# Kernel tuning notes

Measured on AMD Instinct MI355X. Metric: run time of the kernel, lower is better.

The kernel has to match this reference:

```python
import jax, jax.numpy as jnp
import numpy as np

MUL = 32            # multiplicity of 0e and 1o irreps
IN_DIM = MUL * 4    # 32 scalars + 32 vectors = 128
SH_DIM = 4          # 1x0e + 1x1o
N_EDGE_FEAT = 128
HIDDEN = 128
W_NUMEL = 4 * MUL * MUL  # 4 CG paths, uvw weights 32x1x32 each
EPS = 1e-5
INV_SQRT3 = 1.0 / np.sqrt(3.0)
PATH_NORM = 1.0 / np.sqrt(2.0 * MUL)  # 2 paths per output irrep, fan-in MUL


def _fc(edge_attr, W1, b1, W2, b2):
    h = jax.nn.relu(edge_attr @ W1 + b1)
    return h @ W2 + b2  # [E, W_NUMEL]


def _tensor_product(x, sh, w):
    # FullyConnectedTensorProduct for (32x0e+32x1o) x (1x0e+1x1o) -> (32x0e+32x1o)
    # CG (real w3j): 0x0->0: 1 ; 0x1->1, 1x0->1, 1x1->0: delta/sqrt(3)
    E = x.shape[0]
    x0 = x[:, :MUL]                      # [E,32]   scalars
    x1 = x[:, MUL:].reshape(E, MUL, 3)   # [E,32,3] vectors
    sh0 = sh[:, 0]                       # [E]
    sh1 = sh[:, 1:4]                     # [E,3]
    wA = w[:, 0 * MUL * MUL:1 * MUL * MUL].reshape(E, MUL, MUL)  # 0e x 0e -> 0e
    wB = w[:, 1 * MUL * MUL:2 * MUL * MUL].reshape(E, MUL, MUL)  # 0e x 1o -> 1o
    wC = w[:, 2 * MUL * MUL:3 * MUL * MUL].reshape(E, MUL, MUL)  # 1o x 0e -> 1o
    wD = w[:, 3 * MUL * MUL:4 * MUL * MUL].reshape(E, MUL, MUL)  # 1o x 1o -> 0e
    out0 = PATH_NORM * (
        jnp.einsum('eu,euw->ew', x0 * sh0[:, None], wA)
        + INV_SQRT3 * jnp.einsum('eui,ei,euw->ew', x1, sh1, wD))
    out1 = PATH_NORM * INV_SQRT3 * (
        jnp.einsum('eu,ei,euw->ewi', x0, sh1, wB)
        + jnp.einsum('eui,euw->ewi', x1 * sh0[:, None, None], wC))
    return jnp.concatenate([out0, out1.reshape(E, MUL * 3)], axis=-1)  # [E,128]


def _batch_norm(x, bn_weight, bn_bias):
    # e3nn-style equivariant BatchNorm (training stats): scalars get mean/var
    # normalization + affine; vectors get norm normalization + scale.
    N = x.shape[0]
    s = x[:, :MUL]                       # [N,32]
    v = x[:, MUL:].reshape(N, MUL, 3)    # [N,32,3]
    s = s - s.mean(axis=0)
    s = s * (jax.lax.rsqrt((s ** 2).mean(axis=0) + EPS) * bn_weight[:MUL]) + bn_bias
    v_norm = jax.lax.rsqrt((v ** 2).mean(axis=-1).mean(axis=0) + EPS)  # [32]
    v = v * (v_norm * bn_weight[MUL:])[None, :, None]
    return jnp.concatenate([s, v.reshape(N, MUL * 3)], axis=-1)


def _forward(node_attr, edge_index, edge_attr, edge_sh,
             W1, b1, W2, b2, bn_weight, bn_bias):
    edge_src, edge_dst = edge_index[0], edge_index[1]
    N = node_attr.shape[0]
    w = _fc(edge_attr, W1, b1, W2, b2)                     # [E, 4096]
    tp = _tensor_product(node_attr[edge_dst], edge_sh, w)  # [E, 128]
    # scatter mean over edge_src
    summed = jax.ops.segment_sum(tp, edge_src, num_segments=N)
    counts = jax.ops.segment_sum(jnp.ones((tp.shape[0],), tp.dtype), edge_src,
                                 num_segments=N)
    out = summed / jnp.maximum(counts, 1.0)[:, None]
    out = out + node_attr                                  # residual (same dim, pad=0)
    return _batch_norm(out, bn_weight, bn_bias)


def setup_inputs() -> dict:
    key = jax.random.key(0)
    ks = jax.random.split(key, 10)
    N, E = 10000, 60000
    node_attr = jax.random.normal(ks[0], (N, IN_DIM), jnp.float32)
    edge_index = jax.random.randint(ks[1], (2, E), 0, N)
    edge_attr = jax.random.normal(ks[2], (E, N_EDGE_FEAT), jnp.float32)
    edge_sh = jax.random.normal(ks[3], (E, SH_DIM), jnp.float32)
    W1 = jax.random.normal(ks[4], (N_EDGE_FEAT, HIDDEN), jnp.float32) / np.sqrt(N_EDGE_FEAT)
    b1 = jnp.zeros((HIDDEN,), jnp.float32)
    W2 = jax.random.normal(ks[5], (HIDDEN, W_NUMEL), jnp.float32) / np.sqrt(HIDDEN)
    b2 = jnp.zeros((W_NUMEL,), jnp.float32)
    bn_weight = jnp.ones((2 * MUL,), jnp.float32)
    bn_bias = jnp.zeros((MUL,), jnp.float32)
    return {"node_attr": node_attr, "edge_index": edge_index,
            "edge_attr": edge_attr, "edge_sh": edge_sh,
            "W1": W1, "b1": b1, "W2": W2, "b2": b2,
            "bn_weight": bn_weight, "bn_bias": bn_bias}


def reference(node_attr, edge_index, edge_attr, edge_sh,
              W1, b1, W2, b2, bn_weight, bn_bias):
    return _forward(node_attr, edge_index, edge_attr, edge_sh,
                    W1, b1, W2, b2, bn_weight, bn_bias)
```

## Files before the change

### kernel.cpp

```cpp
#include <hip/hip_runtime.h>
#include <math.h>

#define EPSV 1e-5f
#define IS3  0.57735026918962576f
#define PNRM 0.125f

typedef __attribute__((ext_vector_type(8)))  short  short8;
typedef __attribute__((ext_vector_type(16))) float  floatx16;

static __device__ inline unsigned short f2bf(float f) {
    unsigned int u = __float_as_uint(f);
    return (unsigned short)((u + 0x7fff + ((u >> 16) & 1)) >> 16);
}
static __device__ inline float bflo(unsigned int u) { return __uint_as_float(u << 16); }
static __device__ inline float bfhi(unsigned int u) { return __uint_as_float(u & 0xffff0000u); }

#define GLD16(gp, lp) __builtin_amdgcn_global_load_lds( \
    (const __attribute__((address_space(1))) unsigned int*)(gp), \
    (__attribute__((address_space(3))) unsigned int*)(lp), 16, 0, 0)

__global__ __launch_bounds__(256) void k0_tile(const float* __restrict__ W2,
                                               const float* __restrict__ W1,
                                               unsigned short* __restrict__ W2T,
                                               unsigned short* __restrict__ W1T,
                                               const int* __restrict__ ei,
                                               int* __restrict__ deg, int E) {
    const int bx = blockIdx.x, tid = threadIdx.x;
    if (bx >= 132) {
        int e = (bx - 132) * 256 + tid;
        if (e < E) atomicAdd(&deg[ei[e]], 1);
        return;
    }
    __shared__ float tile[128 * 33];
    const float* src;
    unsigned short* dst;
    int nc, tb;
    if (bx < 128) { src = W2; dst = W2T; nc = 4096; tb = bx; }
    else          { src = W1; dst = W1T; nc = 128;  tb = bx - 128; }
    const int c0 = tb * 32;
#pragma unroll
    for (int r = 0; r < 16; ++r) {
        int lin = r * 256 + tid;
        int k = lin >> 5, c = lin & 31;
        tile[k * 33 + c] = src[(size_t)k * nc + c0 + c];
    }
    __syncthreads();
#pragma unroll
    for (int r = 0; r < 2; ++r) {
        int g = r * 256 + tid;
        int kc = g >> 5, c = g & 31;
        short8 v;
#pragma unroll
        for (int j = 0; j < 8; ++j)
            v[j] = (short)f2bf(tile[(kc * 8 + j) * 33 + c]);
        *(short8*)(dst + (size_t)tb * 4096 + kc * 256 + c * 8) = v;
    }
}

__global__ __launch_bounds__(256) void k1_fc(const float* __restrict__ ea,
                                             const unsigned short* __restrict__ W1T,
                                             const float* __restrict__ b1,
                                             unsigned short* __restrict__ hsw,
                                             const int* __restrict__ deg,
                                             int* __restrict__ rowptr,
                                             int N, int E) {
    __shared__ __align__(16) unsigned short W1s[16384];
    __shared__ __align__(16) unsigned short bounce[4 * 1056];
    const int tid = threadIdx.x, lane = tid & 63, wv = tid >> 6;
    const int half = lane >> 5, col = lane & 31;
    const int nfc = (E + 127) / 128;

    if (blockIdx.x >= nfc) {
        int* part = (int*)W1s;
        const int chunk = (N + 255) / 256;
        const int base = tid * chunk;
        int s = 0;
        for (int i = 0; i < chunk; ++i) {
            int n = base + i;
            if (n < N) s += deg[n];
        }
        part[tid] = s;
        __syncthreads();
        for (int off = 1; off < 256; off <<= 1) {
            int t = 0;
            if (tid >= off) t = part[tid - off];
            __syncthreads();
            if (tid >= off) part[tid] += t;
            __syncthreads();
        }
        int prefix = (tid == 0) ? 0 : part[tid - 1];
        for (int i = 0; i < chunk; ++i) {
            int n = base + i;
            if (n < N) { rowptr[n] = prefix; prefix += deg[n]; }
        }
        if (tid == 0) rowptr[N] = part[255];
        return;
    }

    const int e0 = blockIdx.x * 128;

#pragma unroll
    for (int q = 0; q < 8; ++q) {
        int chunk = wv * 8 + q;
        GLD16((const char*)W1T + chunk * 1024 + lane * 16, (char*)W1s + chunk * 1024);
    }

    int e = e0 + wv * 32 + col; if (e >= E) e = E - 1;
    short8 afr[8];
#pragma unroll
    for (int c = 0; c < 8; ++c) {
        const float4* p = (const float4*)(ea + (size_t)e * 128 + c * 16 + half * 8);
        float4 f0 = p[0], f1 = p[1];
        short8 v;
        v[0] = (short)f2bf(f0.x); v[1] = (short)f2bf(f0.y);
        v[2] = (short)f2bf(f0.z); v[3] = (short)f2bf(f0.w);
        v[4] = (short)f2bf(f1.x); v[5] = (short)f2bf(f1.y);
        v[6] = (short)f2bf(f1.z); v[7] = (short)f2bf(f1.w);
        afr[c] = v;
    }
    __syncthreads();

    unsigned short* myb = bounce + wv * 1056;
    const int gg = blockIdx.x * 4 + wv;
#pragma unroll
    for (int jt = 0; jt < 4; ++jt) {
        floatx16 d = {0,0,0,0,0,0,0,0,0,0,0,0,0,0,0,0};
#pragma unroll
        for (int c = 0; c < 8; ++c) {
            short8 bf = *(const short8*)((const char*)W1s + jt * 8192 + (2 * c + half) * 512 + col * 16);
            d = __builtin_amdgcn_mfma_f32_32x32x16_bf16(afr[c], bf, d, 0, 0, 0);
        }
        float b1v = b1[jt * 32 + col];
#pragma unroll
        for (int reg = 0; reg < 16; ++reg) {
            int r = (reg & 3) + 8 * (reg >> 2) + 4 * half;
            float v = d[reg] + b1v;
            v = v > 0.f ? v : 0.f;
            myb[(col >> 3) * 264 + r * 8 + (col & 7)] = f2bf(v);
        }
#pragma unroll
        for (int s = 0; s < 2; ++s) {
            short8 v = *(const short8*)&myb[(s * 2 + (lane >> 5)) * 264 + (lane & 31) * 8];
            *(short8*)(hsw + (size_t)gg * 4096 + jt * 1024 + s * 512 + lane * 8) = v;
        }
    }
}

__global__ __launch_bounds__(256, 2) void k2_mfma(const unsigned short* __restrict__ hsw,
                                                  const unsigned short* __restrict__ W2T,
                                                  const float* __restrict__ b2,
                                                  const float* __restrict__ na,
                                                  const int* __restrict__ ei,
                                                  const float* __restrict__ sh,
                                                  const int* __restrict__ rowptr,
                                                  int* __restrict__ cursor,
                                                  float* __restrict__ tp, int E) {
    __shared__ __align__(16) char smem[32768];
    __shared__ int posbuf[64];
    unsigned short* Ctb = (unsigned short*)smem;
    float* red = (float*)smem;

    const int tid = threadIdx.x, lane = tid & 63, wv = tid >> 6;
    const int half = lane >> 5, col = lane & 31;
    const int ust = wv >> 1, esub = wv & 1;
    const int e0 = blockIdx.x * 64;

    if (tid < 64) {
        int e = e0 + tid;
        if (e < E) {
            int s = ei[e];
            posbuf[tid] = rowptr[s] + atomicAdd(&cursor[s], 1);
        }
    }

    for (int idx = tid; idx < 2048; idx += 256) {
        int el = idx & 63, u = idx >> 6;
        int e = e0 + el; int ec = e < E ? e : E - 1;
        int dn = ei[E + ec];
        const float* nar = na + (size_t)dn * 128;
        float x0  = nar[u];
        float x10 = nar[32 + u * 3], x11 = nar[33 + u * 3], x12 = nar[34 + u * 3];
        const float* shr = sh + (size_t)ec * 4;
        float s0 = shr[0], s1 = shr[1], s2 = shr[2], s3 = shr[3];
        int o = u * 64 + el;
        Ctb[0 * 2048 + o] = f2bf(PNRM * x0 * s0);
        Ctb[1 * 2048 + o] = f2bf(PNRM * IS3 * x0);
        Ctb[2 * 2048 + o] = f2bf(PNRM * IS3 * s0 * x10);
        Ctb[3 * 2048 + o] = f2bf(PNRM * IS3 * s0 * x11);
        Ctb[4 * 2048 + o] = f2bf(PNRM * IS3 * s0 * x12);
        Ctb[5 * 2048 + o] = f2bf(PNRM * IS3 * (x10 * s1 + x11 * s2 + x12 * s3));
    }

    const int gg = blockIdx.x * 2 + esub;
    short8 afr[8];
#pragma unroll
    for (int c = 0; c < 8; ++c)
        afr[c] = *(const short8*)(hsw + (size_t)gg * 4096 + (2 * c + half) * 256 + col * 8);

    __syncthreads();

    float acc0[16] = {}, accB[16] = {}, accC0[16] = {}, accC1[16] = {}, accC2[16] = {};
    const int elb0 = esub * 32 + half * 4;
    const unsigned short* bbase = W2T + half * 256 + col * 8;

#define LOADB(p, br, b2r) do {                                         \
        int _ct = 2 * (p) + ust;                                       \
        const unsigned short* _bp = bbase + (size_t)_ct * 4096;        \
        _Pragma("unroll")                                              \
        for (int _c = 0; _c < 8; ++_c)                                 \
            (br)[_c] = *(const short8*)(_bp + _c * 512);               \
        (b2r) = b2[_ct * 32 + col];                                    \
    } while (0)

#define COMPUTE(p, br, b2v) do {                                                              \
        const int _ct = 2 * (p) + ust;                                                        \
        const int _b = _ct >> 5, _u = _ct & 31;                                               \
        floatx16 d = {0,0,0,0,0,0,0,0,0,0,0,0,0,0,0,0};                                       \
        _Pragma("unroll")                                                                     \
        for (int _c = 0; _c < 8; ++_c)                                                        \
            d = __builtin_amdgcn_mfma_f32_32x32x16_bf16(afr[_c], (br)[_c], d, 0, 0, 0);       \
        if (_b == 0 || _b == 3) {                                                             \
            const unsigned short* tb = Ctb + (_b == 0 ? 0 : 5) * 2048;                        \
            _Pragma("unroll")                                                                 \
            for (int q = 0; q < 4; ++q) {                                                     \
                uint2 cv = *(const uint2*)&tb[_u * 64 + elb0 + q * 8];                        \
                acc0[q * 4 + 0] += bflo(cv.x) * (d[q * 4 + 0] + (b2v));                       \
                acc0[q * 4 + 1] += bfhi(cv.x) * (d[q * 4 + 1] + (b2v));                       \
                acc0[q * 4 + 2] += bflo(cv.y) * (d[q * 4 + 2] + (b2v));                       \
                acc0[q * 4 + 3] += bfhi(cv.y) * (d[q * 4 + 3] + (b2v));                       \
            }                                                                                 \
        } else if (_b == 1) {                                                                 \
            _Pragma("unroll")                                                                 \
            for (int q = 0; q < 4; ++q) {                                                     \
                uint2 cv = *(const uint2*)&Ctb[1 * 2048 + _u * 64 + elb0 + q * 8];            \
                accB[q * 4 + 0] += bflo(cv.x) * (d[q * 4 + 0] + (b2v));                       \
                accB[q * 4 + 1] += bfhi(cv.x) * (d[q * 4 + 1] + (b2v));                       \
                accB[q * 4 + 2] += bflo(cv.y) * (d[q * 4 + 2] + (b2v));                       \
                accB[q * 4 + 3] += bfhi(cv.y) * (d[q * 4 + 3] + (b2v));                       \
            }                                                                                 \
        } else {                                                                              \
            _Pragma("unroll")                                                                 \
            for (int q = 0; q < 4; ++q) {                                                     \
                uint2 cu0 = *(const uint2*)&Ctb[2 * 2048 + _u * 64 + elb0 + q * 8];           \
                uint2 cu1 = *(const uint2*)&Ctb[3 * 2048 + _u * 64 + elb0 + q * 8];           \
                uint2 cu2 = *(const uint2*)&Ctb[4 * 2048 + _u * 64 + elb0 + q * 8];           \
                float f0[4] = {bflo(cu0.x), bfhi(cu0.x), bflo(cu0.y), bfhi(cu0.y)};           \
                float f1[4] = {bflo(cu1.x), bfhi(cu1.x), bflo(cu1.y), bfhi(cu1.y)};           \
                float f2[4] = {bflo(cu2.x), bfhi(cu2.x), bflo(cu2.y), bfhi(cu2.y)};           \
                _Pragma("unroll")                                                             \
                for (int rr = 0; rr < 4; ++rr) {                                              \
                    float v = d[q * 4 + rr] + (b2v);                                          \
                    accC0[q * 4 + rr] += f0[rr] * v;                                          \
                    accC1[q * 4 + rr] += f1[rr] * v;                                          \
                    accC2[q * 4 + rr] += f2[rr] * v;                                          \
                }                                                                             \
            }                                                                                 \
        }                                                                                     \
    } while (0)

    short8 bA[8], bB[8], bC[8];
    float b2A, b2B, b2C;
    LOADB(0, bA, b2A); LOADB(1, bB, b2B); LOADB(2, bC, b2C);
    for (int p = 0; p < 60; p += 3) {
        COMPUTE(p,     bA, b2A); LOADB(p + 3, bA, b2A);
        COMPUTE(p + 1, bB, b2B); LOADB(p + 4, bB, b2B);
        COMPUTE(p + 2, bC, b2C); LOADB(p + 5, bC, b2C);
    }
    COMPUTE(60, bA, b2A); LOADB(63, bA, b2A);
    COMPUTE(61, bB, b2B);
    COMPUTE(62, bC, b2C);
    COMPUTE(63, bA, b2A);
#undef LOADB
#undef COMPUTE

    __syncthreads();
    if (ust == 1) {
#pragma unroll
        for (int q = 0; q < 4; ++q) {
#pragma unroll
            for (int rr = 0; rr < 4; ++rr) {
                int reg = q * 4 + rr;
                int el = esub * 32 + q * 8 + half * 4 + rr;
                int e = e0 + el; int ec = e < E ? e : E - 1;
                float4 sv = *(const float4*)(sh + (size_t)ec * 4);
                red[(((esub * 4 + 0) * 16 + reg) << 6) + lane] = acc0[reg];
                red[(((esub * 4 + 1) * 16 + reg) << 6) + lane] = sv.y * accB[reg] + accC0[reg];
                red[(((esub * 4 + 2) * 16 + reg) << 6) + lane] = sv.z * accB[reg] + accC1[reg];
                red[(((esub * 4 + 3) * 16 + reg) << 6) + lane] = sv.w * accB[reg] + accC2[reg];
            }
        }
    }
    __syncthreads();
    if (ust == 0) {
#pragma unroll
        for (int q = 0; q < 4; ++q) {
#pragma unroll
            for (int rr = 0; rr < 4; ++rr) {
                int reg = q * 4 + rr;
                int el = esub * 32 + q * 8 + half * 4 + rr;
                int e = e0 + el;
                if (e >= E) continue;
                float4 sv = *(const float4*)(sh + (size_t)e * 4);
                float a0 = acc0[reg] + red[(((esub * 4 + 0) * 16 + reg) << 6) + lane];
                float o0 = sv.y * accB[reg] + accC0[reg] + red[(((esub * 4 + 1) * 16 + reg) << 6) + lane];
                float o1 = sv.z * accB[reg] + accC1[reg] + red[(((esub * 4 + 2) * 16 + reg) << 6) + lane];
                float o2 = sv.w * accB[reg] + accC2[reg] + red[(((esub * 4 + 3) * 16 + reg) << 6) + lane];
                float* tpe = tp + (size_t)posbuf[el] * 128;
                tpe[col] = a0;
                tpe[32 + col * 3 + 0] = o0;
                tpe[32 + col * 3 + 1] = o1;
                tpe[32 + col * 3 + 2] = o2;
            }
        }
    }
}

__global__ __launch_bounds__(256) void k4_gather(const float* __restrict__ tp,
                                                 const int* __restrict__ rowptr,
                                                 const float* __restrict__ na,
                                                 float* __restrict__ pre,
                                                 float* __restrict__ stats, int N) {
    __shared__ float bns[96];
    const int tid = threadIdx.x;
    if (tid < 96) bns[tid] = 0.f;
    __syncthreads();
    const int o = tid & 127, hf = tid >> 7;
    for (int n = blockIdx.x * 2 + hf; n < N; n += gridDim.x * 2) {
        int r0 = rowptr[n], r1 = rowptr[n + 1];
        float s = 0.f;
        int j = r0;
        for (; j + 4 <= r1; j += 4) {
            float t0 = tp[(size_t)(j + 0) * 128 + o];
            float t1 = tp[(size_t)(j + 1) * 128 + o];
            float t2 = tp[(size_t)(j + 2) * 128 + o];
            float t3 = tp[(size_t)(j + 3) * 128 + o];
            s += (t0 + t1) + (t2 + t3);
        }
        for (; j < r1; ++j)
            s += tp[(size_t)j * 128 + o];
        int dg = r1 - r0;
        float cf = (float)(dg > 0 ? dg : 1);
        float v = s / cf + na[(size_t)n * 128 + o];
        pre[(size_t)n * 128 + o] = v;
        if (o < 32) {
            atomicAdd(&bns[o], v);
            atomicAdd(&bns[32 + o], v * v);
        } else {
            atomicAdd(&bns[64 + (o - 32) / 3], v * v);
        }
    }
    __syncthreads();
    if (tid < 96) atomicAdd(&stats[tid], bns[tid]);
}

__global__ __launch_bounds__(256) void k5_bn(const float* __restrict__ pre,
                                             const float* __restrict__ stats,
                                             const float* __restrict__ bnw,
                                             const float* __restrict__ bnb,
                                             float* __restrict__ out, int N) {
    size_t idx = (size_t)blockIdx.x * 256 + threadIdx.x;
    if (idx >= (size_t)N * 128) return;
    int o = (int)(idx & 127);
    float v = pre[idx];
    float invN = 1.f / (float)N;
    if (o < 32) {
        float m   = stats[o] * invN;
        float var = stats[32 + o] * invN - m * m;
        out[idx] = (v - m) * rsqrtf(var + EPSV) * bnw[o] + bnb[o];
    } else {
        int j = (o - 32) / 3;
        float vn = rsqrtf(stats[64 + j] * invN * (1.f / 3.f) + EPSV);
        out[idx] = v * vn * bnw[32 + j];
    }
}

extern "C" void kernel_launch(void* const* d_in, const int* in_sizes, int n_in,
                              void* d_out, int out_size, void* d_ws, size_t ws_size,
                              hipStream_t stream) {
    const float* node_attr  = (const float*)d_in[0];
    const int*   edge_index = (const int*)d_in[1];
    const float* edge_attr  = (const float*)d_in[2];
    const float* edge_sh    = (const float*)d_in[3];
    const float* W1  = (const float*)d_in[4];
    const float* b1  = (const float*)d_in[5];
    const float* W2  = (const float*)d_in[6];
    const float* b2  = (const float*)d_in[7];
    const float* bnw = (const float*)d_in[8];
    const float* bnb = (const float*)d_in[9];

    const int N = in_sizes[0] / 128;
    const int E = in_sizes[1] / 2;
    const int ngroups = ((E + 127) / 128) * 4;

    float* tp     = (float*)d_ws;
    float* pre    = tp + (size_t)E * 128;
    float* stats  = pre + (size_t)N * 128;
    int*   deg    = (int*)(stats + 96);
    int*   cursor = deg + N;
    int*   rowptr = cursor + N;
    char* pbase = (char*)(rowptr + N + 1);
    pbase += (16 - ((size_t)pbase & 15)) & 15;
    unsigned short* hsw = (unsigned short*)pbase;
    unsigned short* W2T = hsw + (size_t)ngroups * 4096;
    unsigned short* W1T = W2T + (size_t)524288;

    hipMemsetAsync(stats, 0, (96 + 2 * (size_t)N) * sizeof(int), stream);

    k0_tile<<<132 + (E + 255) / 256, 256, 0, stream>>>(W2, W1, W2T, W1T,
                                                       edge_index, deg, E);
    k1_fc<<<(E + 127) / 128 + 1, 256, 0, stream>>>(edge_attr, W1T, b1, hsw,
                                                   deg, rowptr, N, E);
    k2_mfma<<<(E + 63) / 64, 256, 0, stream>>>(hsw, W2T, b2, node_attr, edge_index,
                                               edge_sh, rowptr, cursor, tp, E);
    k4_gather<<<1024, 256, 0, stream>>>(tp, rowptr, node_attr, pre, stats, N);
    size_t ntot = (size_t)N * 128;
    k5_bn<<<(int)((ntot + 255) / 256), 256, 0, stream>>>(pre, stats, bnw, bnb,
                                                         (float*)d_out, N);
}
```

Before: 255.7 us.

## Fuse gather and batch-norm into one cooperative kernel with grid sync

Merges the per-node gather/mean kernel and the batch-norm apply kernel into one cooperative kernel. Each thread keeps its 16 node values in registers, the block statistics are reduced, a grid-wide barrier follows, and then the normalization is applied directly from registers. This drops the intermediate pre buffer write and reread plus one launch. In exchange it depends on a 512-block cooperative launch, a grid sync, and coverage capped at 16 iterations, so correctness needs N ≤ 16384.

```diff
diff --git a/kernel.cpp b/kernel.cpp
--- a/kernel.cpp
+++ b/kernel.cpp
@@ -1,5 +1,8 @@
 #include <hip/hip_runtime.h>
+#include <hip/hip_cooperative_groups.h>
 #include <math.h>
+
+namespace cg = cooperative_groups;
 
 #define EPSV 1e-5f
 #define IS3  0.57735026918962576f
@@ -315,62 +318,70 @@
     }
 }
 
-__global__ __launch_bounds__(256) void k4_gather(const float* __restrict__ tp,
-                                                 const int* __restrict__ rowptr,
-                                                 const float* __restrict__ na,
-                                                 float* __restrict__ pre,
-                                                 float* __restrict__ stats, int N) {
+__global__ __launch_bounds__(256) void k4c_bn(const float* __restrict__ tp,
+                                              const int* __restrict__ rowptr,
+                                              const float* __restrict__ na,
+                                              float* __restrict__ stats,
+                                              const float* __restrict__ bnw,
+                                              const float* __restrict__ bnb,
+                                              float* __restrict__ out, int N) {
     __shared__ float bns[96];
     const int tid = threadIdx.x;
     if (tid < 96) bns[tid] = 0.f;
     __syncthreads();
     const int o = tid & 127, hf = tid >> 7;
-    for (int n = blockIdx.x * 2 + hf; n < N; n += gridDim.x * 2) {
-        int r0 = rowptr[n], r1 = rowptr[n + 1];
-        float s = 0.f;
-        int j = r0;
-        for (; j + 4 <= r1; j += 4) {
-            float t0 = tp[(size_t)(j + 0) * 128 + o];
-            float t1 = tp[(size_t)(j + 1) * 128 + o];
-            float t2 = tp[(size_t)(j + 2) * 128 + o];
-            float t3 = tp[(size_t)(j + 3) * 128 + o];
-            s += (t0 + t1) + (t2 + t3);
-        }
-        for (; j < r1; ++j)
-            s += tp[(size_t)j * 128 + o];
-        int dg = r1 - r0;
-        float cf = (float)(dg > 0 ? dg : 1);
-        float v = s / cf + na[(size_t)n * 128 + o];
-        pre[(size_t)n * 128 + o] = v;
-        if (o < 32) {
-            atomicAdd(&bns[o], v);
-            atomicAdd(&bns[32 + o], v * v);
-        } else {
-            atomicAdd(&bns[64 + (o - 32) / 3], v * v);
+    const int nbase = blockIdx.x * 2 + hf;
+    const int stride = gridDim.x * 2;
+    float vreg[16];
+#pragma unroll
+    for (int it = 0; it < 16; ++it) {
+        int n = nbase + it * stride;
+        if (n < N) {
+            int r0 = rowptr[n], r1 = rowptr[n + 1];
+            float s = 0.f;
+            int j = r0;
+            for (; j + 4 <= r1; j += 4) {
+                float t0 = tp[(size_t)(j + 0) * 128 + o];
+                float t1 = tp[(size_t)(j + 1) * 128 + o];
+                float t2 = tp[(size_t)(j + 2) * 128 + o];
+                float t3 = tp[(size_t)(j + 3) * 128 + o];
+                s += (t0 + t1) + (t2 + t3);
+            }
+            for (; j < r1; ++j)
+                s += tp[(size_t)j * 128 + o];
+            int dg = r1 - r0;
+            float cf = (float)(dg > 0 ? dg : 1);
+            float v = s / cf + na[(size_t)n * 128 + o];
+            vreg[it] = v;
+            if (o < 32) {
+                atomicAdd(&bns[o], v);
+                atomicAdd(&bns[32 + o], v * v);
+            } else {
+                atomicAdd(&bns[64 + (o - 32) / 3], v * v);
+            }
         }
     }
     __syncthreads();
     if (tid < 96) atomicAdd(&stats[tid], bns[tid]);
-}
-
-__global__ __launch_bounds__(256) void k5_bn(const float* __restrict__ pre,
-                                             const float* __restrict__ stats,
-                                             const float* __restrict__ bnw,
-                                             const float* __restrict__ bnb,
-                                             float* __restrict__ out, int N) {
-    size_t idx = (size_t)blockIdx.x * 256 + threadIdx.x;
-    if (idx >= (size_t)N * 128) return;
-    int o = (int)(idx & 127);
-    float v = pre[idx];
+
+    cg::this_grid().sync();
+
     float invN = 1.f / (float)N;
+    float scale, bias;
     if (o < 32) {
         float m   = stats[o] * invN;
         float var = stats[32 + o] * invN - m * m;
-        out[idx] = (v - m) * rsqrtf(var + EPSV) * bnw[o] + bnb[o];
+        float is  = rsqrtf(var + EPSV) * bnw[o];
+        scale = is; bias = bnb[o] - m * is;
     } else {
-        int j = (o - 32) / 3;
-        float vn = rsqrtf(stats[64 + j] * invN * (1.f / 3.f) + EPSV);
-        out[idx] = v * vn * bnw[32 + j];
+        int jj = (o - 32) / 3;
+        scale = rsqrtf(stats[64 + jj] * invN * (1.f / 3.f) + EPSV) * bnw[32 + jj];
+        bias = 0.f;
+    }
+#pragma unroll
+    for (int it = 0; it < 16; ++it) {
+        int n = nbase + it * stride;
+        if (n < N) out[(size_t)n * 128 + o] = vreg[it] * scale + bias;
     }
 }
 
@@ -393,8 +404,7 @@
     const int ngroups = ((E + 127) / 128) * 4;
 
     float* tp     = (float*)d_ws;
-    float* pre    = tp + (size_t)E * 128;
-    float* stats  = pre + (size_t)N * 128;
+    float* stats  = tp + (size_t)E * 128;
     int*   deg    = (int*)(stats + 96);
     int*   cursor = deg + N;
     int*   rowptr = cursor + N;
@@ -412,8 +422,9 @@
                                                    deg, rowptr, N, E);
     k2_mfma<<<(E + 63) / 64, 256, 0, stream>>>(hsw, W2T, b2, node_attr, edge_index,
                                                edge_sh, rowptr, cursor, tp, E);
-    k4_gather<<<1024, 256, 0, stream>>>(tp, rowptr, node_attr, pre, stats, N);
-    size_t ntot = (size_t)N * 128;
-    k5_bn<<<(int)((ntot + 255) / 256), 256, 0, stream>>>(pre, stats, bnw, bnb,
-                                                         (float*)d_out, N);
-}
+
+    float* outf = (float*)d_out;
+    void* kargs[] = {(void*)&tp, (void*)&rowptr, (void*)&node_attr, (void*)&stats,
+                     (void*)&bnw, (void*)&bnb, (void*)&outf, (void*)&N};
+    hipLaunchCooperativeKernel((void*)k4c_bn, dim3(512), dim3(256), kargs, 0, stream);
+}
```

Measured after the change: 308.3 us. +20.6%, slower.

## Shrink FC kernel to one-wave blocks reading W1 directly from global

Applied to the files above, without the earlier changes.

Restructures k1_fc from 256-thread blocks that stage the whole bf16 W1T into LDS into 64-thread single-wave blocks that read W1T fragments straight from global/L2 for the MFMA B operand. The degree prefix scan now runs in one wave with shuffle-up instead of a 256-thread LDS scan with barriers, so it uses 64 lanes with larger chunks. This removes the LDS staging and block-wide barriers and raises occupancy. In exchange every wave refetches W1T from cache, and the serial scan work per lane grows.

```diff
diff --git a/kernel.cpp b/kernel.cpp
--- a/kernel.cpp
+++ b/kernel.cpp
@@ -14,10 +14,6 @@
 }
 static __device__ inline float bflo(unsigned int u) { return __uint_as_float(u << 16); }
 static __device__ inline float bfhi(unsigned int u) { return __uint_as_float(u & 0xffff0000u); }
-
-#define GLD16(gp, lp) __builtin_amdgcn_global_load_lds( \
-    (const __attribute__((address_space(1))) unsigned int*)(gp), \
-    (__attribute__((address_space(3))) unsigned int*)(lp), 16, 0, 0)
 
 __global__ __launch_bounds__(256) void k0_tile(const float* __restrict__ W2,
                                                const float* __restrict__ W1,
@@ -57,55 +53,44 @@
     }
 }
 
-__global__ __launch_bounds__(256) void k1_fc(const float* __restrict__ ea,
-                                             const unsigned short* __restrict__ W1T,
-                                             const float* __restrict__ b1,
-                                             unsigned short* __restrict__ hsw,
-                                             const int* __restrict__ deg,
-                                             int* __restrict__ rowptr,
-                                             int N, int E) {
-    __shared__ __align__(16) unsigned short W1s[16384];
-    __shared__ __align__(16) unsigned short bounce[4 * 1056];
-    const int tid = threadIdx.x, lane = tid & 63, wv = tid >> 6;
+__global__ __launch_bounds__(64) void k1_fc(const float* __restrict__ ea,
+                                            const unsigned short* __restrict__ W1T,
+                                            const float* __restrict__ b1,
+                                            unsigned short* __restrict__ hsw,
+                                            const int* __restrict__ deg,
+                                            int* __restrict__ rowptr,
+                                            int N, int E) {
+    const int lane = threadIdx.x & 63;
     const int half = lane >> 5, col = lane & 31;
-    const int nfc = (E + 127) / 128;
+    const int nfc = (E + 31) / 32;
 
     if (blockIdx.x >= nfc) {
-        int* part = (int*)W1s;
-        const int chunk = (N + 255) / 256;
-        const int base = tid * chunk;
+        const int chunk = (N + 63) / 64;
+        const int base = lane * chunk;
         int s = 0;
         for (int i = 0; i < chunk; ++i) {
             int n = base + i;
             if (n < N) s += deg[n];
         }
-        part[tid] = s;
-        __syncthreads();
-        for (int off = 1; off < 256; off <<= 1) {
-            int t = 0;
-            if (tid >= off) t = part[tid - off];
-            __syncthreads();
-            if (tid >= off) part[tid] += t;
-            __syncthreads();
-        }
-        int prefix = (tid == 0) ? 0 : part[tid - 1];
+        int inc = s;
+#pragma unroll
+        for (int off = 1; off < 64; off <<= 1) {
+            int t = __shfl_up(inc, off);
+            if (lane >= off) inc += t;
+        }
+        int prefix = inc - s;
         for (int i = 0; i < chunk; ++i) {
             int n = base + i;
             if (n < N) { rowptr[n] = prefix; prefix += deg[n]; }
         }
-        if (tid == 0) rowptr[N] = part[255];
+        if (lane == 63) rowptr[N] = inc;
         return;
     }
 
-    const int e0 = blockIdx.x * 128;
-
-#pragma unroll
-    for (int q = 0; q < 8; ++q) {
-        int chunk = wv * 8 + q;
-        GLD16((const char*)W1T + chunk * 1024 + lane * 16, (char*)W1s + chunk * 1024);
-    }
-
-    int e = e0 + wv * 32 + col; if (e >= E) e = E - 1;
+    __shared__ __align__(16) unsigned short myb[1056];
+    const int e0 = blockIdx.x * 32;
+
+    int e = e0 + col; if (e >= E) e = E - 1;
     short8 afr[8];
 #pragma unroll
     for (int c = 0; c < 8; ++c) {
@@ -118,16 +103,14 @@
         v[6] = (short)f2bf(f1.z); v[7] = (short)f2bf(f1.w);
         afr[c] = v;
     }
-    __syncthreads();
-
-    unsigned short* myb = bounce + wv * 1056;
-    const int gg = blockIdx.x * 4 + wv;
+
+    const int gg = blockIdx.x;
 #pragma unroll
     for (int jt = 0; jt < 4; ++jt) {
         floatx16 d = {0,0,0,0,0,0,0,0,0,0,0,0,0,0,0,0};
 #pragma unroll
         for (int c = 0; c < 8; ++c) {
-            short8 bf = *(const short8*)((const char*)W1s + jt * 8192 + (2 * c + half) * 512 + col * 16);
+            short8 bf = *(const short8*)((const char*)W1T + jt * 8192 + (2 * c + half) * 512 + col * 16);
             d = __builtin_amdgcn_mfma_f32_32x32x16_bf16(afr[c], bf, d, 0, 0, 0);
         }
         float b1v = b1[jt * 32 + col];
@@ -408,8 +391,8 @@
 
     k0_tile<<<132 + (E + 255) / 256, 256, 0, stream>>>(W2, W1, W2T, W1T,
                                                        edge_index, deg, E);
-    k1_fc<<<(E + 127) / 128 + 1, 256, 0, stream>>>(edge_attr, W1T, b1, hsw,
-                                                   deg, rowptr, N, E);
+    k1_fc<<<(E + 31) / 32 + 1, 64, 0, stream>>>(edge_attr, W1T, b1, hsw,
+                                                deg, rowptr, N, E);
     k2_mfma<<<(E + 63) / 64, 256, 0, stream>>>(hsw, W2T, b2, node_attr, edge_index,
                                                edge_sh, rowptr, cursor, tp, E);
     k4_gather<<<1024, 256, 0, stream>>>(tp, rowptr, node_attr, pre, stats, N);
```

Measured after the change: 296.7 us. 1.16x slower.
